# Performance work log

Hardware: AMD Instinct MI355X
Metric: run time of the kernel (lower is better)

Reference implementation:

```python
import jax, jax.numpy as jnp
import numpy as np

EPS = 1e-12

def _natural_vvg_sym(x):
    """Natural vector visibility graph for one example.
    x: [S, D]. Returns symmetric 0/1 adjacency [S, S] = vg + vg.T (vg upper-triangular).
    Node a sees node b (a<b) iff for all a<c<b:
        y_c < y_b + (y_a - y_b) * (b - c) / (b - a),  y_k = <x_k, x_b> / ||x_b||
    """
    S = x.shape[0]
    t = jnp.arange(S, dtype=x.dtype)
    norms = jnp.maximum(jnp.linalg.norm(x, axis=-1), EPS)        # [S]
    Y = (x @ x.T) / norms[:, None]                                # Y[b,c] = <x_c,x_b>/||x_b||
    d = jnp.diagonal(Y)                                           # y_b = ||x_b||, [S]
    ta = t[:, None, None]   # a axis
    tb = t[None, :, None]   # b axis
    tc = t[None, None, :]   # c axis
    denom = jnp.where(tb != ta, tb - ta, jnp.ones((), x.dtype))   # avoid 0/0 on diagonal
    # visibility line at time c for pair (a,b): [S,S,S] indexed [a,b,c]
    line = d[None, :, None] + (Y.T[:, :, None] - d[None, :, None]) * (tb - tc) / denom
    between = (tc > ta) & (tc < tb)                               # strict interior points
    blocked = jnp.any((Y[None, :, :] >= line) & between, axis=-1) # [a,b]
    upper = t[None, :] > t[:, None]                               # b > a
    vg = (upper & ~blocked).astype(x.dtype)                       # upper-triangular adjacency
    return vg + vg.T


def setup_inputs() -> dict:
    key = jax.random.key(0)
    k1, k2 = jax.random.split(key)
    token_embs = jax.random.normal(k1, (8, 256, 768), dtype=jnp.float32)
    W = jax.random.normal(k2, (768, 4), dtype=jnp.float32)
    return {"token_embs": token_embs, "W": W}


def reference(token_embs, W):
    # vg_sym: [B, S, S]
    vg_sym = jax.vmap(_natural_vvg_sym)(token_embs)
    # torch: out[i] = multi_dot([vg, example, W])[0] == vg_sym[0] @ example @ W
    row0 = vg_sym[:, 0, :]                          # [B, S]
    h = jnp.einsum('bs,bsd->bd', row0, token_embs)  # [B, 768]
    logits = h @ W                                  # [B, n_class]
    return jax.nn.log_softmax(logits, axis=-1)
```

## Files before the change

kernel.cpp:

```cpp
#include <hip/hip_runtime.h>
#include <hip/hip_bf16.h>

constexpr int S  = 256;
constexpr int D  = 768;
constexpr int KQ = 8;
constexpr int KS = D / KQ;
constexpr int GROWS = KQ * S;

typedef _Float16 half8  __attribute__((ext_vector_type(8)));
typedef _Float16 half4v __attribute__((ext_vector_type(4)));
typedef float    f32x4  __attribute__((ext_vector_type(4)));

__device__ const int TI_MAP[10] = {0,1,1,2,2,2,3,3,3,3};
__device__ const int TJ_MAP[10] = {0,0,1,0,1,2,0,1,2,3};

__global__ __launch_bounds__(256) void gram_kernel(const float* __restrict__ X,
                                                   const float* __restrict__ Wm,
                                                   float* __restrict__ G,
                                                   float* __restrict__ Ppart) {
    const int ti    = TI_MAP[blockIdx.x];
    const int tj    = TJ_MAP[blockIdx.x];
    const int batch = blockIdx.y;
    const int kq    = blockIdx.z;
    const bool diag = (ti == tj);

    const float* Xq = X + (size_t)batch * S * D + kq * KS;

    __shared__ _Float16 AhS[64][104], AlS[64][104], BhS[64][104], BlS[64][104];
    __shared__ float Ws[96][4];

    const int t    = threadIdx.x;
    const int srow = t >> 2;
    const int sk   = (t & 3) * 24;

    if (diag && t < 96)
        *(float4*)&Ws[t][0] = *(const float4*)(Wm + (size_t)(kq * KS + t) * 4);

    const float* pa = Xq + (size_t)(ti * 64 + srow) * D + sk;
    const float* pb = Xq + (size_t)(tj * 64 + srow) * D + sk;

    float4 xva[6];
#pragma unroll
    for (int c = 0; c < 6; ++c) {
        const int ko = sk + c * 4;
        const float4 va = *(const float4*)(pa + c * 4);
        xva[c] = va;
        half4v ha, la;
        ha.x = (_Float16)va.x; la.x = (_Float16)(va.x - (float)ha.x);
        ha.y = (_Float16)va.y; la.y = (_Float16)(va.y - (float)ha.y);
        ha.z = (_Float16)va.z; la.z = (_Float16)(va.z - (float)ha.z);
        ha.w = (_Float16)va.w; la.w = (_Float16)(va.w - (float)ha.w);
        *(half4v*)&AhS[srow][ko] = ha;
        *(half4v*)&AlS[srow][ko] = la;
    }
    if (!diag) {
#pragma unroll
        for (int c = 0; c < 6; ++c) {
            const int ko = sk + c * 4;
            const float4 vb = *(const float4*)(pb + c * 4);
            half4v hb, lb;
            hb.x = (_Float16)vb.x; lb.x = (_Float16)(vb.x - (float)hb.x);
            hb.y = (_Float16)vb.y; lb.y = (_Float16)(vb.y - (float)hb.y);
            hb.z = (_Float16)vb.z; lb.z = (_Float16)(vb.z - (float)hb.z);
            hb.w = (_Float16)vb.w; lb.w = (_Float16)(vb.w - (float)hb.w);
            *(half4v*)&BhS[srow][ko] = hb;
            *(half4v*)&BlS[srow][ko] = lb;
        }
    }
    __syncthreads();

    if (diag) {
        float4 pacc = make_float4(0.f, 0.f, 0.f, 0.f);
#pragma unroll
        for (int c = 0; c < 6; ++c) {
            const float xf[4] = {xva[c].x, xva[c].y, xva[c].z, xva[c].w};
#pragma unroll
            for (int q = 0; q < 4; ++q) {
                const float4 wq = *(const float4*)&Ws[sk + c * 4 + q][0];
                pacc.x = fmaf(xf[q], wq.x, pacc.x);
                pacc.y = fmaf(xf[q], wq.y, pacc.y);
                pacc.z = fmaf(xf[q], wq.z, pacc.z);
                pacc.w = fmaf(xf[q], wq.w, pacc.w);
            }
        }
#pragma unroll
        for (int off = 1; off <= 2; off <<= 1) {
            pacc.x += __shfl_xor(pacc.x, off);
            pacc.y += __shfl_xor(pacc.y, off);
            pacc.z += __shfl_xor(pacc.z, off);
            pacc.w += __shfl_xor(pacc.w, off);
        }
        if ((t & 3) == 0)
            *(float4*)(Ppart + (((size_t)batch * S + ti * 64 + srow) * KQ + kq) * 4) = pacc;
    }

    _Float16 (*Bh)[104] = diag ? AhS : BhS;
    _Float16 (*Bl)[104] = diag ? AlS : BlS;

    const int lane = t & 63;
    const int w    = t >> 6;
    const int frow = lane & 15;
    const int fko  = (lane >> 4) * 8;

    f32x4 acc[4] = {};
#pragma unroll
    for (int ks = 0; ks < 3; ++ks) {
        const int k0 = ks * 32 + fko;
        const half8 ah = *(const half8*)&AhS[w * 16 + frow][k0];
        const half8 al = *(const half8*)&AlS[w * 16 + frow][k0];
#pragma unroll
        for (int n = 0; n < 4; ++n) {
            const half8 bh = *(const half8*)&Bh[n * 16 + frow][k0];
            const half8 bl = *(const half8*)&Bl[n * 16 + frow][k0];
            acc[n] = __builtin_amdgcn_mfma_f32_16x16x32_f16(ah, bh, acc[n], 0, 0, 0);
            acc[n] = __builtin_amdgcn_mfma_f32_16x16x32_f16(ah, bl, acc[n], 0, 0, 0);
            acc[n] = __builtin_amdgcn_mfma_f32_16x16x32_f16(al, bh, acc[n], 0, 0, 0);
        }
    }

    float* gout = G + ((size_t)(batch * S + ti * 64 + w * 16 + (lane >> 4) * 4) * KQ + kq) * S
                    + tj * 64 + frow;
#pragma unroll
    for (int n = 0; n < 4; ++n)
#pragma unroll
        for (int r = 0; r < 4; ++r)
            gout[(size_t)r * GROWS + n * 16] = acc[n][r];
}

__global__ __launch_bounds__(256) void vis_kernel(const float* __restrict__ G,
                                                  float* __restrict__ wv) {
    const int batch = blockIdx.y;
    const int wave  = threadIdx.x >> 6;
    const int lane  = threadIdx.x & 63;
    const int b     = blockIdx.x * 4 + wave;

    const float* rbp = G + (size_t)(batch * S + b) * GROWS + 4 * lane;
    float4 s0 = make_float4(0.f, 0.f, 0.f, 0.f), s1 = s0, s2 = s0, s3 = s0;
    if (4 * lane <= b) {
#pragma unroll
        for (int sl = 0; sl < 2; ++sl) {
            const float4 v0 = *(const float4*)(rbp + (size_t)(4 * sl + 0) * S);
            const float4 v1 = *(const float4*)(rbp + (size_t)(4 * sl + 1) * S);
            const float4 v2 = *(const float4*)(rbp + (size_t)(4 * sl + 2) * S);
            const float4 v3 = *(const float4*)(rbp + (size_t)(4 * sl + 3) * S);
            s0.x += v0.x; s0.y += v0.y; s0.z += v0.z; s0.w += v0.w;
            s1.x += v1.x; s1.y += v1.y; s1.z += v1.z; s1.w += v1.w;
            s2.x += v2.x; s2.y += v2.y; s2.z += v2.z; s2.w += v2.w;
            s3.x += v3.x; s3.y += v3.y; s3.z += v3.z; s3.w += v3.w;
        }
    }
    float4 gs;
    gs.x = (s0.x + s1.x) + (s2.x + s3.x);
    gs.y = (s0.y + s1.y) + (s2.y + s3.y);
    gs.z = (s0.z + s1.z) + (s2.z + s3.z);
    gs.w = (s0.w + s1.w) + (s2.w + s3.w);

    const int bq = b & 3;
    float sel = (bq == 0) ? gs.x : ((bq == 1) ? gs.y : ((bq == 2) ? gs.z : gs.w));
    const float gb = __shfl(sel, b >> 2);
    const float g0 = __shfl(gs.x, 0);
    const float denom = (b > 0) ? (float)b : 1.0f;

    bool blocked = false;
    {
        const int c0 = 4 * lane;
#define VTEST(Q, GV) { const int c = c0 + (Q); \
        const float line = gb + ((g0 - gb) * (float)(b - c)) / denom; \
        if (c >= 1 && c < b && (GV) >= line) blocked = true; }
        VTEST(0, gs.x) VTEST(1, gs.y) VTEST(2, gs.z) VTEST(3, gs.w)
#undef VTEST
    }
    const bool visflag = (b >= 1) && !__any(blocked);

    if (lane == 0) wv[batch * S + b] = visflag ? 1.0f : 0.0f;
}

__global__ __launch_bounds__(256) void head_kernel(const float* __restrict__ Ppart,
                                                   const float* __restrict__ wv,
                                                   float* __restrict__ out) {
    const int batch = blockIdx.x;
    const int t     = threadIdx.x;
    const int wave  = t >> 6;
    const int lane  = t & 63;

    float4 acc = make_float4(0.f, 0.f, 0.f, 0.f);
    if (wv[batch * S + t] != 0.0f) {
        const float* pp = Ppart + ((size_t)batch * S + t) * (KQ * 4);
#pragma unroll
        for (int kq = 0; kq < KQ; ++kq) {
            const float4 p = *(const float4*)(pp + kq * 4);
            acc.x += p.x; acc.y += p.y; acc.z += p.z; acc.w += p.w;
        }
    }
#pragma unroll
    for (int off = 32; off; off >>= 1) {
        acc.x += __shfl_xor(acc.x, off);
        acc.y += __shfl_xor(acc.y, off);
        acc.z += __shfl_xor(acc.z, off);
        acc.w += __shfl_xor(acc.w, off);
    }

    __shared__ float4 lsh[4];
    if (lane == 0) lsh[wave] = acc;
    __syncthreads();

    if (t == 0) {
        const float l0 = ((lsh[0].x + lsh[1].x) + (lsh[2].x + lsh[3].x));
        const float l1 = ((lsh[0].y + lsh[1].y) + (lsh[2].y + lsh[3].y));
        const float l2 = ((lsh[0].z + lsh[1].z) + (lsh[2].z + lsh[3].z));
        const float l3 = ((lsh[0].w + lsh[1].w) + (lsh[2].w + lsh[3].w));
        const float m = fmaxf(fmaxf(l0, l1), fmaxf(l2, l3));
        const float lse = logf(expf(l0 - m) + expf(l1 - m) + expf(l2 - m) + expf(l3 - m));
        out[batch * 4 + 0] = l0 - m - lse;
        out[batch * 4 + 1] = l1 - m - lse;
        out[batch * 4 + 2] = l2 - m - lse;
        out[batch * 4 + 3] = l3 - m - lse;
    }
}

extern "C" void kernel_launch(void* const* d_in, const int* in_sizes, int n_in,
                              void* d_out, int out_size, void* d_ws, size_t ws_size,
                              hipStream_t stream) {
    const float* X  = (const float*)d_in[0];
    const float* Wm = (const float*)d_in[1];
    float* out = (float*)d_out;

    float* ws = (float*)d_ws;
    float* Ppart = ws;
    float* wv    = ws + 65536;
    float* G     = ws + 65536 + 2048;

    gram_kernel<<<dim3(10, 8, 8), 256, 0, stream>>>(X, Wm, G, Ppart);
    vis_kernel <<<dim3(64, 8),    256, 0, stream>>>(G, wv);
    head_kernel<<<8,              256, 0, stream>>>(Ppart, wv, out);
}
```

Measured before the change: 19.69 us.

## Halve K-split count and loop two K-chunks per gram block with prefetch

```diff
diff --git a/kernel.cpp b/kernel.cpp
--- a/kernel.cpp
+++ b/kernel.cpp
@@ -3,8 +3,9 @@
 
 constexpr int S  = 256;
 constexpr int D  = 768;
-constexpr int KQ = 8;
+constexpr int KQ = 4;
 constexpr int KS = D / KQ;
+constexpr int CH = 96;
 constexpr int GROWS = KQ * S;
 
 typedef _Float16 half8  __attribute__((ext_vector_type(8)));
@@ -27,62 +28,121 @@
     const float* Xq = X + (size_t)batch * S * D + kq * KS;
 
     __shared__ _Float16 AhS[64][104], AlS[64][104], BhS[64][104], BlS[64][104];
-    __shared__ float Ws[96][4];
+    __shared__ float Ws[192][4];
 
     const int t    = threadIdx.x;
     const int srow = t >> 2;
     const int sk   = (t & 3) * 24;
 
-    if (diag && t < 96)
+    if (diag && t < 192)
         *(float4*)&Ws[t][0] = *(const float4*)(Wm + (size_t)(kq * KS + t) * 4);
 
     const float* pa = Xq + (size_t)(ti * 64 + srow) * D + sk;
     const float* pb = Xq + (size_t)(tj * 64 + srow) * D + sk;
 
-    float4 xva[6];
-#pragma unroll
-    for (int c = 0; c < 6; ++c) {
-        const int ko = sk + c * 4;
-        const float4 va = *(const float4*)(pa + c * 4);
-        xva[c] = va;
-        half4v ha, la;
-        ha.x = (_Float16)va.x; la.x = (_Float16)(va.x - (float)ha.x);
-        ha.y = (_Float16)va.y; la.y = (_Float16)(va.y - (float)ha.y);
-        ha.z = (_Float16)va.z; la.z = (_Float16)(va.z - (float)ha.z);
-        ha.w = (_Float16)va.w; la.w = (_Float16)(va.w - (float)ha.w);
-        *(half4v*)&AhS[srow][ko] = ha;
-        *(half4v*)&AlS[srow][ko] = la;
-    }
+    float4 va[6], vb[6], xva[6];
+#pragma unroll
+    for (int c = 0; c < 6; ++c) va[c] = *(const float4*)(pa + c * 4);
     if (!diag) {
+#pragma unroll
+        for (int c = 0; c < 6; ++c) vb[c] = *(const float4*)(pb + c * 4);
+    }
+
+    const int lane = t & 63;
+    const int w    = t >> 6;
+    const int rb   = (w >> 1) * 32;
+    const int cb   = (w & 1) * 32;
+    const int frow = lane & 15;
+    const int fko  = (lane >> 4) * 8;
+
+    f32x4 acc00 = {}, acc01 = {}, acc10 = {}, acc11 = {};
+    float4 pacc = make_float4(0.f, 0.f, 0.f, 0.f);
+
+    for (int ch = 0; ch < 2; ++ch) {
+        if (ch) __syncthreads();
 #pragma unroll
         for (int c = 0; c < 6; ++c) {
             const int ko = sk + c * 4;
-            const float4 vb = *(const float4*)(pb + c * 4);
-            half4v hb, lb;
-            hb.x = (_Float16)vb.x; lb.x = (_Float16)(vb.x - (float)hb.x);
-            hb.y = (_Float16)vb.y; lb.y = (_Float16)(vb.y - (float)hb.y);
-            hb.z = (_Float16)vb.z; lb.z = (_Float16)(vb.z - (float)hb.z);
-            hb.w = (_Float16)vb.w; lb.w = (_Float16)(vb.w - (float)hb.w);
-            *(half4v*)&BhS[srow][ko] = hb;
-            *(half4v*)&BlS[srow][ko] = lb;
-        }
-    }
-    __syncthreads();
+            const float4 a = va[c];
+            half4v ha, la;
+            ha.x = (_Float16)a.x; la.x = (_Float16)(a.x - (float)ha.x);
+            ha.y = (_Float16)a.y; la.y = (_Float16)(a.y - (float)ha.y);
+            ha.z = (_Float16)a.z; la.z = (_Float16)(a.z - (float)ha.z);
+            ha.w = (_Float16)a.w; la.w = (_Float16)(a.w - (float)ha.w);
+            *(half4v*)&AhS[srow][ko] = ha;
+            *(half4v*)&AlS[srow][ko] = la;
+        }
+        if (!diag) {
+#pragma unroll
+            for (int c = 0; c < 6; ++c) {
+                const int ko = sk + c * 4;
+                const float4 bq = vb[c];
+                half4v hb, lb;
+                hb.x = (_Float16)bq.x; lb.x = (_Float16)(bq.x - (float)hb.x);
+                hb.y = (_Float16)bq.y; lb.y = (_Float16)(bq.y - (float)hb.y);
+                hb.z = (_Float16)bq.z; lb.z = (_Float16)(bq.z - (float)hb.z);
+                hb.w = (_Float16)bq.w; lb.w = (_Float16)(bq.w - (float)hb.w);
+                *(half4v*)&BhS[srow][ko] = hb;
+                *(half4v*)&BlS[srow][ko] = lb;
+            }
+        } else {
+#pragma unroll
+            for (int c = 0; c < 6; ++c) xva[c] = va[c];
+        }
+        if (ch == 0) {
+#pragma unroll
+            for (int c = 0; c < 6; ++c) va[c] = *(const float4*)(pa + CH + c * 4);
+            if (!diag) {
+#pragma unroll
+                for (int c = 0; c < 6; ++c) vb[c] = *(const float4*)(pb + CH + c * 4);
+            }
+        }
+        __syncthreads();
+
+        if (diag) {
+#pragma unroll
+            for (int c = 0; c < 6; ++c) {
+                const float xf[4] = {xva[c].x, xva[c].y, xva[c].z, xva[c].w};
+#pragma unroll
+                for (int q = 0; q < 4; ++q) {
+                    const float4 wq = *(const float4*)&Ws[ch * CH + sk + c * 4 + q][0];
+                    pacc.x = fmaf(xf[q], wq.x, pacc.x);
+                    pacc.y = fmaf(xf[q], wq.y, pacc.y);
+                    pacc.z = fmaf(xf[q], wq.z, pacc.z);
+                    pacc.w = fmaf(xf[q], wq.w, pacc.w);
+                }
+            }
+        }
+
+        _Float16 (*Bh)[104] = diag ? AhS : BhS;
+        _Float16 (*Bl)[104] = diag ? AlS : BlS;
+#pragma unroll
+        for (int ks = 0; ks < 3; ++ks) {
+            const int k0 = ks * 32 + fko;
+            const half8 ah0 = *(const half8*)&AhS[rb + frow][k0];
+            const half8 al0 = *(const half8*)&AlS[rb + frow][k0];
+            const half8 ah1 = *(const half8*)&AhS[rb + 16 + frow][k0];
+            const half8 al1 = *(const half8*)&AlS[rb + 16 + frow][k0];
+            const half8 bh0 = *(const half8*)&Bh[cb + frow][k0];
+            const half8 bl0 = *(const half8*)&Bl[cb + frow][k0];
+            const half8 bh1 = *(const half8*)&Bh[cb + 16 + frow][k0];
+            const half8 bl1 = *(const half8*)&Bl[cb + 16 + frow][k0];
+            acc00 = __builtin_amdgcn_mfma_f32_16x16x32_f16(ah0, bh0, acc00, 0, 0, 0);
+            acc00 = __builtin_amdgcn_mfma_f32_16x16x32_f16(ah0, bl0, acc00, 0, 0, 0);
+            acc00 = __builtin_amdgcn_mfma_f32_16x16x32_f16(al0, bh0, acc00, 0, 0, 0);
+            acc01 = __builtin_amdgcn_mfma_f32_16x16x32_f16(ah0, bh1, acc01, 0, 0, 0);
+            acc01 = __builtin_amdgcn_mfma_f32_16x16x32_f16(ah0, bl1, acc01, 0, 0, 0);
+            acc01 = __builtin_amdgcn_mfma_f32_16x16x32_f16(al0, bh1, acc01, 0, 0, 0);
+            acc10 = __builtin_amdgcn_mfma_f32_16x16x32_f16(ah1, bh0, acc10, 0, 0, 0);
+            acc10 = __builtin_amdgcn_mfma_f32_16x16x32_f16(ah1, bl0, acc10, 0, 0, 0);
+            acc10 = __builtin_amdgcn_mfma_f32_16x16x32_f16(al1, bh0, acc10, 0, 0, 0);
+            acc11 = __builtin_amdgcn_mfma_f32_16x16x32_f16(ah1, bh1, acc11, 0, 0, 0);
+            acc11 = __builtin_amdgcn_mfma_f32_16x16x32_f16(ah1, bl1, acc11, 0, 0, 0);
+            acc11 = __builtin_amdgcn_mfma_f32_16x16x32_f16(al1, bh1, acc11, 0, 0, 0);
+        }
+    }
 
     if (diag) {
-        float4 pacc = make_float4(0.f, 0.f, 0.f, 0.f);
-#pragma unroll
-        for (int c = 0; c < 6; ++c) {
-            const float xf[4] = {xva[c].x, xva[c].y, xva[c].z, xva[c].w};
-#pragma unroll
-            for (int q = 0; q < 4; ++q) {
-                const float4 wq = *(const float4*)&Ws[sk + c * 4 + q][0];
-                pacc.x = fmaf(xf[q], wq.x, pacc.x);
-                pacc.y = fmaf(xf[q], wq.y, pacc.y);
-                pacc.z = fmaf(xf[q], wq.z, pacc.z);
-                pacc.w = fmaf(xf[q], wq.w, pacc.w);
-            }
-        }
 #pragma unroll
         for (int off = 1; off <= 2; off <<= 1) {
             pacc.x += __shfl_xor(pacc.x, off);
@@ -94,37 +154,15 @@
             *(float4*)(Ppart + (((size_t)batch * S + ti * 64 + srow) * KQ + kq) * 4) = pacc;
     }
 
-    _Float16 (*Bh)[104] = diag ? AhS : BhS;
-    _Float16 (*Bl)[104] = diag ? AlS : BlS;
-
-    const int lane = t & 63;
-    const int w    = t >> 6;
-    const int frow = lane & 15;
-    const int fko  = (lane >> 4) * 8;
-
-    f32x4 acc[4] = {};
-#pragma unroll
-    for (int ks = 0; ks < 3; ++ks) {
-        const int k0 = ks * 32 + fko;
-        const half8 ah = *(const half8*)&AhS[w * 16 + frow][k0];
-        const half8 al = *(const half8*)&AlS[w * 16 + frow][k0];
-#pragma unroll
-        for (int n = 0; n < 4; ++n) {
-            const half8 bh = *(const half8*)&Bh[n * 16 + frow][k0];
-            const half8 bl = *(const half8*)&Bl[n * 16 + frow][k0];
-            acc[n] = __builtin_amdgcn_mfma_f32_16x16x32_f16(ah, bh, acc[n], 0, 0, 0);
-            acc[n] = __builtin_amdgcn_mfma_f32_16x16x32_f16(ah, bl, acc[n], 0, 0, 0);
-            acc[n] = __builtin_amdgcn_mfma_f32_16x16x32_f16(al, bh, acc[n], 0, 0, 0);
-        }
-    }
-
-    float* gout = G + ((size_t)(batch * S + ti * 64 + w * 16 + (lane >> 4) * 4) * KQ + kq) * S
-                    + tj * 64 + frow;
-#pragma unroll
-    for (int n = 0; n < 4; ++n)
-#pragma unroll
-        for (int r = 0; r < 4; ++r)
-            gout[(size_t)r * GROWS + n * 16] = acc[n][r];
+    float* gout = G + ((size_t)(batch * S + ti * 64 + rb + (lane >> 4) * 4) * KQ + kq) * S
+                    + tj * 64 + cb + frow;
+#pragma unroll
+    for (int r = 0; r < 4; ++r) {
+        gout[(size_t)r * GROWS]                    = acc00[r];
+        gout[(size_t)r * GROWS + 16]               = acc01[r];
+        gout[(size_t)(16 + r) * GROWS]             = acc10[r];
+        gout[(size_t)(16 + r) * GROWS + 16]        = acc11[r];
+    }
 }
 
 __global__ __launch_bounds__(256) void vis_kernel(const float* __restrict__ G,
@@ -137,17 +175,10 @@
     const float* rbp = G + (size_t)(batch * S + b) * GROWS + 4 * lane;
     float4 s0 = make_float4(0.f, 0.f, 0.f, 0.f), s1 = s0, s2 = s0, s3 = s0;
     if (4 * lane <= b) {
-#pragma unroll
-        for (int sl = 0; sl < 2; ++sl) {
-            const float4 v0 = *(const float4*)(rbp + (size_t)(4 * sl + 0) * S);
-            const float4 v1 = *(const float4*)(rbp + (size_t)(4 * sl + 1) * S);
-            const float4 v2 = *(const float4*)(rbp + (size_t)(4 * sl + 2) * S);
-            const float4 v3 = *(const float4*)(rbp + (size_t)(4 * sl + 3) * S);
-            s0.x += v0.x; s0.y += v0.y; s0.z += v0.z; s0.w += v0.w;
-            s1.x += v1.x; s1.y += v1.y; s1.z += v1.z; s1.w += v1.w;
-            s2.x += v2.x; s2.y += v2.y; s2.z += v2.z; s2.w += v2.w;
-            s3.x += v3.x; s3.y += v3.y; s3.z += v3.z; s3.w += v3.w;
-        }
+        s0 = *(const float4*)(rbp + (size_t)0 * S);
+        s1 = *(const float4*)(rbp + (size_t)1 * S);
+        s2 = *(const float4*)(rbp + (size_t)2 * S);
+        s3 = *(const float4*)(rbp + (size_t)3 * S);
     }
     float4 gs;
     gs.x = (s0.x + s1.x) + (s2.x + s3.x);
@@ -227,10 +258,10 @@
 
     float* ws = (float*)d_ws;
     float* Ppart = ws;
-    float* wv    = ws + 65536;
-    float* G     = ws + 65536 + 2048;
-
-    gram_kernel<<<dim3(10, 8, 8), 256, 0, stream>>>(X, Wm, G, Ppart);
+    float* wv    = ws + 32768;
+    float* G     = ws + 34816;
+
+    gram_kernel<<<dim3(10, 8, 4), 256, 0, stream>>>(X, Wm, G, Ppart);
     vis_kernel <<<dim3(64, 8),    256, 0, stream>>>(G, wv);
     head_kernel<<<8,              256, 0, stream>>>(Ppart, wv, out);
 }
```

Result: faster. 18.27 us (-7.2%).
